# Kernel tuning notes

Measured on AMD Instinct MI355X. Metric: run time of the kernel, lower is better.

Reference implementation:

```python
import jax, jax.numpy as jnp
import numpy as np

NEG = -1000000.0  # same finite mask value as the Triton kernel


def setup_inputs() -> dict:
    key = jax.random.key(0)
    k1, k2, k3, k4 = jax.random.split(key, 4)
    B, H, KVH, S, D = 1, 32, 8, 2048, 128
    return {
        "q": jax.random.normal(k1, (B, H, S, D), dtype=jnp.float32),
        "k": jax.random.normal(k2, (B, KVH, S, D), dtype=jnp.float32),
        "v": jax.random.normal(k3, (B, KVH, S, D), dtype=jnp.float32),
        "sinks": jax.random.normal(k4, (H,), dtype=jnp.float32),
        "bandwidth": 1024,
    }


def reference(q, k, v, sinks, bandwidth):
    """Prefill flash attention with causal + sliding-window masking, GQA, and
    per-head attention sinks (extra logit in the softmax denominator)."""
    B, H, S, D = q.shape
    ratio = H // k.shape[1]  # KV_HEAD_RATIO
    kf = jnp.repeat(k, ratio, axis=1)  # [B,H,S,D]
    vf = jnp.repeat(v, ratio, axis=1)
    sm_scale = 1.0 / np.sqrt(D).astype(np.float32)

    logits = jnp.einsum("bhqd,bhkd->bhqk", q, kf) * sm_scale  # [B,H,S,S]
    q_pos = jnp.arange(S)[:, None]
    k_pos = jnp.arange(S)[None, :]
    mask = k_pos > q_pos  # causal
    if bandwidth > 0:
        mask = mask | (k_pos < q_pos - bandwidth + 1)  # sliding window
    logits = jnp.where(mask, NEG, logits)

    sink = sinks[None, :, None]  # [1,H,1] broadcast over batch, query
    m = jnp.maximum(jnp.max(logits, axis=-1), sink)  # [B,H,S]
    p = jnp.exp(logits - m[..., None])
    denom = p.sum(axis=-1) + jnp.exp(sink - m)  # sink contributes to denom only
    out = jnp.einsum("bhqk,bhkd->bhqd", p, vf) / denom[..., None]
    return out
```

## Files before the change

### kernel.cpp

```cpp
#include <hip/hip_runtime.h>
#include <hip/hip_bf16.h>

typedef __bf16 bf16x8 __attribute__((ext_vector_type(8)));
typedef unsigned short u16x8 __attribute__((ext_vector_type(8)));
typedef unsigned int u32x4 __attribute__((ext_vector_type(4)));
typedef float f32x4 __attribute__((ext_vector_type(4)));

#define SLEN 2048
#define DDIM 128
#define NH   32
#define NKVH 8
#define KVB  32
#define MINIT  -1e30f
#define MASKED -3e30f
#define LOG2E  1.4426950408889634f

static __device__ __forceinline__ unsigned short f2bfu(float f) {
  union { float f; unsigned u; } x; x.f = f;
  return (unsigned short)((x.u + 0x7fffu + ((x.u >> 16) & 1u)) >> 16);
}
static __device__ __forceinline__ float bfu2f(unsigned short u) {
  union { unsigned u; float f; } x; x.u = ((unsigned)u) << 16;
  return x.f;
}
static __device__ __forceinline__ unsigned cvt_pk_bf16(float lo, float hi) {
  unsigned r;
  asm("v_cvt_pk_bf16_f32 %0, %1, %2" : "=v"(r) : "v"(lo), "v"(hi));
  return r;
}
static __device__ __forceinline__ f32x4 mfma_bf16(u16x8 a, u16x8 b, f32x4 c) {
  return __builtin_amdgcn_mfma_f32_16x16x32_bf16(
      __builtin_bit_cast(bf16x8, a), __builtin_bit_cast(bf16x8, b), c, 0, 0, 0);
}
static __device__ __forceinline__ int vswz_k(int row) {
  return (row & 3) | (((row >> 3) & 1) << 2);
}

__global__ __launch_bounds__(256) void conv_kv(const float* __restrict__ k,
                                               const float* __restrict__ v,
                                               unsigned* __restrict__ kdst,
                                               unsigned short* __restrict__ vt) {
  __shared__ unsigned T32[32][17];
  const int bb = blockIdx.x;
  if (bb < 1024) {
    const int i = bb * 256 + threadIdx.x;
    const float4 f0 = ((const float4*)k)[2 * i];
    const float4 f1 = ((const float4*)k)[2 * i + 1];
    u32x4 o = { cvt_pk_bf16(f0.x, f0.y), cvt_pk_bf16(f0.z, f0.w),
                cvt_pk_bf16(f1.x, f1.y), cvt_pk_bf16(f1.z, f1.w) };
    ((u32x4*)kdst)[i] = o;
    return;
  }
  const int b   = bb - 1024;
  const int dt  = b & 3;
  const int st  = (b >> 2) & 63;
  const int kvh = b >> 8;
  const int r  = threadIdx.x >> 3;
  const int cg = threadIdx.x & 7;
  const float4 f = *(const float4*)(v + ((size_t)(kvh * SLEN + st * 32 + r) * DDIM) + dt * 32 + cg * 4);
  T32[r][cg * 2]     = cvt_pk_bf16(f.x, f.y);
  T32[r][cg * 2 + 1] = cvt_pk_bf16(f.z, f.w);
  __syncthreads();
  const int dr = threadIdx.x >> 3;
  const unsigned sel = (dr & 1) ? 0x07060302u : 0x05040100u;
  const unsigned a0 = T32[cg * 4 + 0][dr >> 1], a1 = T32[cg * 4 + 1][dr >> 1];
  const unsigned a2 = T32[cg * 4 + 2][dr >> 1], a3 = T32[cg * 4 + 3][dr >> 1];
  unsigned short* vp = vt + (size_t)kvh * DDIM * SLEN + (size_t)(dt * 32 + dr) * SLEN + st * 32 + cg * 4;
  const unsigned w0 = __builtin_amdgcn_perm(a1, a0, sel);
  const unsigned w1 = __builtin_amdgcn_perm(a3, a2, sel);
  vp[0] = (unsigned short)(w0 & 0xffff);
  vp[1] = (unsigned short)(w0 >> 16);
  vp[2] = (unsigned short)(w1 & 0xffff);
  vp[3] = (unsigned short)(w1 >> 16);
}

template <int NCH>
__global__ __launch_bounds__(256, 4) void attn_fwd(
    const float* __restrict__ q, const unsigned short* __restrict__ kbf,
    const unsigned short* __restrict__ vtg, const float* __restrict__ sinks,
    const int* __restrict__ bwp, float* __restrict__ out,
    unsigned short* __restrict__ pO, float* __restrict__ pm,
    float* __restrict__ pl) {
  constexpr int NQT = 32;
  __shared__ unsigned short Kl[KVB * DDIM];
  __shared__ unsigned short Vt[DDIM * KVB];
  __shared__ float SmS[4][16];

  const int tid  = threadIdx.x;
  const int wid  = tid >> 6;
  const int lane = tid & 63;
  const int ln   = lane & 15;
  const int hi   = lane >> 4;

  const int B   = blockIdx.x;
  const int x   = B & 7;
  const int j   = B >> 3;
  constexpr int per = 4 * NCH;
  const int qt  = NQT - 1 - (j / per);
  const int rem = j % per;
  const int hh  = rem / NCH;
  const int c   = rem % NCH;
  const int h   = x * 4 + hh;
  const int kvh = x;
  const int q0  = qt * 64;
  const int qrow0 = q0 + wid * 16;
  const int qpos  = qrow0 + ln;

  const int bwv    = bwp[0];
  const int lo_off = (bwv > 0) ? (bwv - 1) : SLEN;

  const int T0 = max(0, q0 - lo_off) >> 5;
  const int T1 = (q0 + 63) >> 5;
  const int N  = T1 - T0 + 1;
  const int ch = (N + NCH - 1) / NCH;
  const int Ts = T0 + c * ch;
  const int Te = min(T1, Ts + ch - 1);

  const float c2 = 0.08838834764831845f * LOG2E;

  u16x8 qf[4];
  {
    const float* qp = q + ((size_t)(h * SLEN + qpos) * DDIM) + hi * 8;
    #pragma unroll
    for (int dk = 0; dk < 4; ++dk) {
      float4 f0 = *(const float4*)(qp + dk * 32);
      float4 f1 = *(const float4*)(qp + dk * 32 + 4);
      u32x4 t = { cvt_pk_bf16(f0.x, f0.y), cvt_pk_bf16(f0.z, f0.w),
                  cvt_pk_bf16(f1.x, f1.y), cvt_pk_bf16(f1.z, f1.w) };
      qf[dk] = __builtin_bit_cast(u16x8, t);
    }
  }

  float m2 = MINIT;
  float l_ln = 0.0f;
  f32x4 oacc[8];
  #pragma unroll
  for (int nt = 0; nt < 8; ++nt) oacc[nt] = f32x4{0.f, 0.f, 0.f, 0.f};

  const unsigned short* Kg = kbf + (size_t)kvh * SLEN * DDIM;
  const unsigned short* Vg = vtg + (size_t)kvh * DDIM * SLEN;

  const int kr0 = tid >> 4, sk = tid & 15;
  const int kr1 = kr0 + 16;
  const int kw0 = kr0 * DDIM + (((sk & 8) | ((sk & 7) ^ vswz_k(kr0))) * 8);
  const int kw1 = kr1 * DDIM + (((sk & 8) | ((sk & 7) ^ vswz_k(kr1))) * 8);
  const int vr0 = tid >> 2, sv = tid & 3;
  const int vr1 = vr0 + 64;
  const int vw0 = vr0 * KVB + ((sv ^ ((vr0 >> 1) & 3)) * 8);
  const int vw1 = vr1 * KVB + ((sv ^ ((vr1 >> 1) & 3)) * 8);

  const int prow = ((ln >> 2) << 3) | (ln & 3);
  const int vk   = (ln & 3) | (((ln >> 2) & 1) << 2);
  int kfo[4];
  #pragma unroll
  for (int dk = 0; dk < 4; ++dk) {
    const int s = dk * 4 + hi;
    kfo[dk] = prow * DDIM + (((s & 8) | ((s & 7) ^ vk)) * 8);
  }
  const int vro = ln * KVB + ((hi ^ ((ln >> 1) & 3)) * 8);

  if (Ts <= Te) {
    const int kbS = Ts * 32, kbE = Te * 32;

    u16x8 pk0, pk1, pv0, pv1;
    {
      pk0 = *(const u16x8*)(Kg + (size_t)(kbS + kr0) * DDIM + sk * 8);
      pk1 = *(const u16x8*)(Kg + (size_t)(kbS + kr1) * DDIM + sk * 8);
      pv0 = *(const u16x8*)(Vg + (size_t)vr0 * SLEN + kbS + sv * 8);
      pv1 = *(const u16x8*)(Vg + (size_t)vr1 * SLEN + kbS + sv * 8);
    }

    for (int kb = kbS; kb <= kbE; kb += KVB) {
      __syncthreads();
      *(u16x8*)&Kl[kw0] = pk0;
      *(u16x8*)&Kl[kw1] = pk1;
      *(u16x8*)&Vt[vw0] = pv0;
      *(u16x8*)&Vt[vw1] = pv1;
      __syncthreads();

      {
        const int nb = min(kb + KVB, kbE);
        pk0 = *(const u16x8*)(Kg + (size_t)(nb + kr0) * DDIM + sk * 8);
        pk1 = *(const u16x8*)(Kg + (size_t)(nb + kr1) * DDIM + sk * 8);
        pv0 = *(const u16x8*)(Vg + (size_t)vr0 * SLEN + nb + sv * 8);
        pv1 = *(const u16x8*)(Vg + (size_t)vr1 * SLEN + nb + sv * 8);
      }

      if (kb > qrow0 + 15) continue;
      if (kb + KVB - 1 < qrow0 - lo_off) continue;

      f32x4 sacc0 = {0,0,0,0}, sacc1 = {0,0,0,0};
      __builtin_amdgcn_s_setprio(1);
      #pragma unroll
      for (int dk = 0; dk < 4; ++dk) {
        sacc0 = mfma_bf16(*(const u16x8*)&Kl[kfo[dk]], qf[dk], sacc0);
        sacc1 = mfma_bf16(*(const u16x8*)&Kl[kfo[dk] + 4 * DDIM], qf[dk], sacc1);
      }
      __builtin_amdgcn_s_setprio(0);

      float p[8];
      const bool interior = (kb + KVB - 1 <= qrow0) && (kb >= qrow0 + 15 - lo_off);
      if (interior) {
        #pragma unroll
        for (int r = 0; r < 4; ++r) {
          p[r]     = sacc0[r] * c2;
          p[4 + r] = sacc1[r] * c2;
        }
      } else {
        #pragma unroll
        for (int r = 0; r < 4; ++r) {
          const int kp0 = kb + hi * 8 + r;
          const int kp1 = kp0 + 4;
          p[r]     = ((kp0 <= qpos) && (kp0 >= qpos - lo_off)) ? sacc0[r] * c2 : MASKED;
          p[4 + r] = ((kp1 <= qpos) && (kp1 >= qpos - lo_off)) ? sacc1[r] * c2 : MASKED;
        }
      }

      float mx = fmaxf(fmaxf(fmaxf(p[0], p[1]), fmaxf(p[2], p[3])),
                       fmaxf(fmaxf(p[4], p[5]), fmaxf(p[6], p[7])));
      mx = fmaxf(mx, __shfl_xor(mx, 16));
      mx = fmaxf(mx, __shfl_xor(mx, 32));

      if (__any(mx > m2 + 11.5415605f)) {
        const float mn   = fmaxf(m2, mx);
        const float corr = exp2f(m2 - mn);
        l_ln *= corr;
        m2 = mn;
        if (hi == 0) SmS[wid][ln] = corr;
        float c4[4];
        #pragma unroll
        for (int r = 0; r < 4; ++r) c4[r] = SmS[wid][hi * 4 + r];
        #pragma unroll
        for (int nt = 0; nt < 8; ++nt)
          #pragma unroll
          for (int r = 0; r < 4; ++r) oacc[nt][r] *= c4[r];
      }

      float s = 0.0f;
      #pragma unroll
      for (int jj = 0; jj < 8; ++jj) { p[jj] = exp2f(p[jj] - m2); s += p[jj]; }
      l_ln += s;

      const u32x4 paw = { cvt_pk_bf16(p[0], p[1]), cvt_pk_bf16(p[2], p[3]),
                          cvt_pk_bf16(p[4], p[5]), cvt_pk_bf16(p[6], p[7]) };
      const u16x8 pa = __builtin_bit_cast(u16x8, paw);

      __builtin_amdgcn_s_setprio(1);
      #pragma unroll
      for (int nt = 0; nt < 8; ++nt) {
        const u16x8 vb = *(const u16x8*)&Vt[vro + nt * 16 * KVB];
        oacc[nt] = mfma_bf16(pa, vb, oacc[nt]);
      }
      __builtin_amdgcn_s_setprio(0);
    }
  }

  l_ln += __shfl_xor(l_ln, 16);
  l_ln += __shfl_xor(l_ln, 32);

  if (NCH == 1) {
    const float sk2 = sinks[h] * LOG2E;
    const float M  = fmaxf(m2, sk2);
    const float ed = exp2f(m2 - M);
    const float fac_ln = ed / (l_ln * ed + exp2f(sk2 - M));
    if (hi == 0) SmS[wid][ln] = fac_ln;
    float fac4[4];
    #pragma unroll
    for (int r = 0; r < 4; ++r) fac4[r] = SmS[wid][hi * 4 + r];
    #pragma unroll
    for (int r = 0; r < 4; ++r) {
      float* op = out + ((size_t)(h * SLEN + qrow0 + hi*4 + r) * DDIM) + ln;
      #pragma unroll
      for (int nt = 0; nt < 8; ++nt) op[nt * 16] = oacc[nt][r] * fac4[r];
    }
  } else {
    const size_t Lb = ((size_t)(h * NQT + qt)) * NCH + c;
    if (hi == 0) {
      pm[Lb * 64 + wid * 16 + ln] = m2;
      pl[Lb * 64 + wid * 16 + ln] = l_ln;
    }
    #pragma unroll
    for (int r = 0; r < 4; ++r) {
      unsigned short* po = pO + (Lb * 64 + wid * 16 + hi * 4 + r) * 128 + ln;
      #pragma unroll
      for (int nt = 0; nt < 8; ++nt) po[nt * 16] = f2bfu(oacc[nt][r]);
    }
  }
}

template <int NCH, int QBLK, int NQT>
__global__ __launch_bounds__(256) void mergeN(
    const unsigned short* __restrict__ pO, const float* __restrict__ pm,
    const float* __restrict__ pl, const float* __restrict__ sinks,
    float* __restrict__ out) {
  const int b   = blockIdx.x;
  const int x   = b & 7;
  const int jj2 = b >> 3;
  const int h   = x * 4 + (jj2 >> 5);
  const int sub = jj2 & 31;
  const int rloc = sub * 64 + (threadIdx.x >> 2);
  const int rid  = h * 2048 + rloc;
  const int d0   = (threadIdx.x & 3) * 32;
  const int qt   = rloc / QBLK;
  const int lr   = rloc % QBLK;
  const size_t base = ((size_t)(h * NQT + qt) * NCH) * QBLK + lr;
  const float sk2 = sinks[h] * LOG2E;
  float mc[NCH], lc[NCH];
  float M = sk2;
  #pragma unroll
  for (int c = 0; c < NCH; ++c) {
    mc[c] = pm[base + (size_t)c * QBLK];
    lc[c] = pl[base + (size_t)c * QBLK];
    M = fmaxf(M, mc[c]);
  }
  float denom = exp2f(sk2 - M);
  float sc[NCH];
  #pragma unroll
  for (int c = 0; c < NCH; ++c) { sc[c] = exp2f(mc[c] - M); denom += lc[c] * sc[c]; }
  const float inv = 1.0f / denom;
  float o[32];
  #pragma unroll
  for (int i = 0; i < 32; ++i) o[i] = 0.f;
  #pragma unroll
  for (int c = 0; c < NCH; ++c) {
    const unsigned short* pp = pO + (base + (size_t)c * QBLK) * 128 + d0;
    const float s = sc[c] * inv;
    #pragma unroll
    for (int i = 0; i < 4; ++i) {
      u16x8 a = *(const u16x8*)(pp + i * 8);
      #pragma unroll
      for (int jj = 0; jj < 8; ++jj) o[i*8+jj] += bfu2f(a[jj]) * s;
    }
  }
  float* op = out + (size_t)rid * 128 + d0;
  #pragma unroll
  for (int i = 0; i < 8; ++i)
    *(float4*)(op + i*4) = make_float4(o[i*4], o[i*4+1], o[i*4+2], o[i*4+3]);
}

extern "C" void kernel_launch(void* const* d_in, const int* in_sizes, int n_in,
                              void* d_out, int out_size, void* d_ws, size_t ws_size,
                              hipStream_t stream) {
  const float* q     = (const float*)d_in[0];
  const float* k     = (const float*)d_in[1];
  const float* v     = (const float*)d_in[2];
  const float* sinks = (const float*)d_in[3];
  const int*   bw    = (const int*)d_in[4];
  float* out = (float*)d_out;

  const size_t kvElems = (size_t)NKVH * SLEN * DDIM;
  unsigned short* kbf = (unsigned short*)d_ws;
  unsigned short* vtg = kbf + kvElems;
  unsigned short* pO  = vtg + kvElems;

  const size_t nPart2 = (size_t)NH * 32 * 2 * 64;
  const size_t need2  = 4 * kvElems + nPart2 * 128 * 2 + nPart2 * 8;

  conv_kv<<<dim3(1024 + NKVH * 64 * 4), 256, 0, stream>>>(k, v, (unsigned*)kbf, vtg);

  if (ws_size >= need2) {
    float* pm = (float*)(pO + nPart2 * 128);
    float* pl = pm + nPart2;
    attn_fwd<2><<<dim3(2048), 256, 0, stream>>>(q, kbf, vtg, sinks, bw, out, pO, pm, pl);
    mergeN<2, 64, 32><<<dim3(1024), 256, 0, stream>>>(pO, pm, pl, sinks, out);
  } else {
    attn_fwd<1><<<dim3(1024), 256, 0, stream>>>(q, kbf, vtg, sinks, bw, out, pO, nullptr, nullptr);
  }
}
```

Baseline: 75.37 us.

## Switch attention to 32x32x16 MFMA with 128-row query tiles

Replaces the 16x16x32 bf16 MFMA tiling with 32x32x16 MFMA. Each wave now owns 32 query rows, so the block covers a 128-row query tile and the grid is halved. The K and V LDS layouts change to match the new operand format, and v_permlane32_swap repacks the P fragments for the PV product. The aim is to reuse each K/V tile across more query rows and issue fewer, larger MFMAs, at the cost of more registers (occupancy hint lowered from 4 to 2), fewer blocks and coarser causal/window tiles that waste more masked work.

```diff
diff --git a/kernel.cpp b/kernel.cpp
--- a/kernel.cpp
+++ b/kernel.cpp
@@ -4,7 +4,7 @@
 typedef __bf16 bf16x8 __attribute__((ext_vector_type(8)));
 typedef unsigned short u16x8 __attribute__((ext_vector_type(8)));
 typedef unsigned int u32x4 __attribute__((ext_vector_type(4)));
-typedef float f32x4 __attribute__((ext_vector_type(4)));
+typedef float f32x16 __attribute__((ext_vector_type(16)));
 
 #define SLEN 2048
 #define DDIM 128
@@ -28,12 +28,12 @@
   asm("v_cvt_pk_bf16_f32 %0, %1, %2" : "=v"(r) : "v"(lo), "v"(hi));
   return r;
 }
-static __device__ __forceinline__ f32x4 mfma_bf16(u16x8 a, u16x8 b, f32x4 c) {
-  return __builtin_amdgcn_mfma_f32_16x16x32_bf16(
+static __device__ __forceinline__ f32x16 mfma32(u16x8 a, u16x8 b, f32x16 c) {
+  return __builtin_amdgcn_mfma_f32_32x32x16_bf16(
       __builtin_bit_cast(bf16x8, a), __builtin_bit_cast(bf16x8, b), c, 0, 0, 0);
 }
-static __device__ __forceinline__ int vswz_k(int row) {
-  return (row & 3) | (((row >> 3) & 1) << 2);
+static __device__ __forceinline__ void plswap(unsigned &a, unsigned &b) {
+  asm volatile("v_permlane32_swap_b32 %0, %1" : "+v"(a), "+v"(b));
 }
 
 __global__ __launch_bounds__(256) void conv_kv(const float* __restrict__ k,
@@ -75,22 +75,23 @@
 }
 
 template <int NCH>
-__global__ __launch_bounds__(256, 4) void attn_fwd(
+__global__ __launch_bounds__(256, 2) void attn_fwd(
     const float* __restrict__ q, const unsigned short* __restrict__ kbf,
     const unsigned short* __restrict__ vtg, const float* __restrict__ sinks,
     const int* __restrict__ bwp, float* __restrict__ out,
     unsigned short* __restrict__ pO, float* __restrict__ pm,
     float* __restrict__ pl) {
-  constexpr int NQT = 32;
-  __shared__ unsigned short Kl[KVB * DDIM];
-  __shared__ unsigned short Vt[DDIM * KVB];
-  __shared__ float SmS[4][16];
+  constexpr int QBLK = 128;
+  constexpr int NQT  = SLEN / QBLK;
+  __shared__ unsigned short Kt[16 * 32 * 8];
+  __shared__ unsigned short Vt2[4 * 128 * 8];
+  __shared__ float SmS[4][32];
 
   const int tid  = threadIdx.x;
   const int wid  = tid >> 6;
   const int lane = tid & 63;
-  const int ln   = lane & 15;
-  const int hi   = lane >> 4;
+  const int qc   = lane & 31;
+  const int hf   = lane >> 5;
 
   const int B   = blockIdx.x;
   const int x   = B & 7;
@@ -102,15 +103,15 @@
   const int c   = rem % NCH;
   const int h   = x * 4 + hh;
   const int kvh = x;
-  const int q0  = qt * 64;
-  const int qrow0 = q0 + wid * 16;
-  const int qpos  = qrow0 + ln;
+  const int q0  = qt * QBLK;
+  const int qrow0 = q0 + wid * 32;
+  const int qpos  = qrow0 + qc;
 
   const int bwv    = bwp[0];
   const int lo_off = (bwv > 0) ? (bwv - 1) : SLEN;
 
   const int T0 = max(0, q0 - lo_off) >> 5;
-  const int T1 = (q0 + 63) >> 5;
+  const int T1 = (q0 + QBLK - 1) >> 5;
   const int N  = T1 - T0 + 1;
   const int ch = (N + NCH - 1) / NCH;
   const int Ts = T0 + c * ch;
@@ -118,13 +119,13 @@
 
   const float c2 = 0.08838834764831845f * LOG2E;
 
-  u16x8 qf[4];
+  u16x8 qf[8];
   {
-    const float* qp = q + ((size_t)(h * SLEN + qpos) * DDIM) + hi * 8;
-    #pragma unroll
-    for (int dk = 0; dk < 4; ++dk) {
-      float4 f0 = *(const float4*)(qp + dk * 32);
-      float4 f1 = *(const float4*)(qp + dk * 32 + 4);
+    const float* qp = q + ((size_t)(h * SLEN + qpos) * DDIM) + hf * 8;
+    #pragma unroll
+    for (int dk = 0; dk < 8; ++dk) {
+      float4 f0 = *(const float4*)(qp + dk * 16);
+      float4 f1 = *(const float4*)(qp + dk * 16 + 4);
       u32x4 t = { cvt_pk_bf16(f0.x, f0.y), cvt_pk_bf16(f0.z, f0.w),
                   cvt_pk_bf16(f1.x, f1.y), cvt_pk_bf16(f1.z, f1.w) };
       qf[dk] = __builtin_bit_cast(u16x8, t);
@@ -133,92 +134,83 @@
 
   float m2 = MINIT;
   float l_ln = 0.0f;
-  f32x4 oacc[8];
-  #pragma unroll
-  for (int nt = 0; nt < 8; ++nt) oacc[nt] = f32x4{0.f, 0.f, 0.f, 0.f};
+  f32x16 oacc[4];
+  #pragma unroll
+  for (int t = 0; t < 4; ++t)
+    #pragma unroll
+    for (int r = 0; r < 16; ++r) oacc[t][r] = 0.0f;
 
   const unsigned short* Kg = kbf + (size_t)kvh * SLEN * DDIM;
   const unsigned short* Vg = vtg + (size_t)kvh * DDIM * SLEN;
 
-  const int kr0 = tid >> 4, sk = tid & 15;
-  const int kr1 = kr0 + 16;
-  const int kw0 = kr0 * DDIM + (((sk & 8) | ((sk & 7) ^ vswz_k(kr0))) * 8);
-  const int kw1 = kr1 * DDIM + (((sk & 8) | ((sk & 7) ^ vswz_k(kr1))) * 8);
-  const int vr0 = tid >> 2, sv = tid & 3;
-  const int vr1 = vr0 + 64;
-  const int vw0 = vr0 * KVB + ((sv ^ ((vr0 >> 1) & 3)) * 8);
-  const int vw1 = vr1 * KVB + ((sv ^ ((vr1 >> 1) & 3)) * 8);
-
-  const int prow = ((ln >> 2) << 3) | (ln & 3);
-  const int vk   = (ln & 3) | (((ln >> 2) & 1) << 2);
-  int kfo[4];
-  #pragma unroll
-  for (int dk = 0; dk < 4; ++dk) {
-    const int s = dk * 4 + hi;
-    kfo[dk] = prow * DDIM + (((s & 8) | ((s & 7) ^ vk)) * 8);
-  }
-  const int vro = ln * KVB + ((hi ^ ((ln >> 1) & 3)) * 8);
+  const int i0 = tid, i1 = 256 + tid;
+  const int ks0 = i0 >> 5, kr0 = i0 & 31;
+  const int ks1 = i1 >> 5, kr1 = i1 & 31;
+  const int vs0 = i0 >> 7, vd0 = i0 & 127;
+  const int vs1 = i1 >> 7, vd1 = i1 & 127;
+  const int klo0 = ks0 * 256 + kr0 * 8, klo1 = ks1 * 256 + kr1 * 8;
+  const int vlo0 = vs0 * 1024 + vd0 * 8, vlo1 = vs1 * 1024 + vd1 * 8;
+
+  int kro[8];
+  #pragma unroll
+  for (int dk = 0; dk < 8; ++dk) kro[dk] = (dk * 2 + hf) * 256 + qc * 8;
 
   if (Ts <= Te) {
     const int kbS = Ts * 32, kbE = Te * 32;
 
     u16x8 pk0, pk1, pv0, pv1;
-    {
-      pk0 = *(const u16x8*)(Kg + (size_t)(kbS + kr0) * DDIM + sk * 8);
-      pk1 = *(const u16x8*)(Kg + (size_t)(kbS + kr1) * DDIM + sk * 8);
-      pv0 = *(const u16x8*)(Vg + (size_t)vr0 * SLEN + kbS + sv * 8);
-      pv1 = *(const u16x8*)(Vg + (size_t)vr1 * SLEN + kbS + sv * 8);
-    }
+    pk0 = *(const u16x8*)(Kg + (size_t)(kbS + kr0) * DDIM + ks0 * 8);
+    pk1 = *(const u16x8*)(Kg + (size_t)(kbS + kr1) * DDIM + ks1 * 8);
+    pv0 = *(const u16x8*)(Vg + (size_t)vd0 * SLEN + kbS + vs0 * 8);
+    pv1 = *(const u16x8*)(Vg + (size_t)vd1 * SLEN + kbS + vs1 * 8);
 
     for (int kb = kbS; kb <= kbE; kb += KVB) {
       __syncthreads();
-      *(u16x8*)&Kl[kw0] = pk0;
-      *(u16x8*)&Kl[kw1] = pk1;
-      *(u16x8*)&Vt[vw0] = pv0;
-      *(u16x8*)&Vt[vw1] = pv1;
+      *(u16x8*)&Kt[klo0]  = pk0;
+      *(u16x8*)&Kt[klo1]  = pk1;
+      *(u16x8*)&Vt2[vlo0] = pv0;
+      *(u16x8*)&Vt2[vlo1] = pv1;
       __syncthreads();
 
       {
         const int nb = min(kb + KVB, kbE);
-        pk0 = *(const u16x8*)(Kg + (size_t)(nb + kr0) * DDIM + sk * 8);
-        pk1 = *(const u16x8*)(Kg + (size_t)(nb + kr1) * DDIM + sk * 8);
-        pv0 = *(const u16x8*)(Vg + (size_t)vr0 * SLEN + nb + sv * 8);
-        pv1 = *(const u16x8*)(Vg + (size_t)vr1 * SLEN + nb + sv * 8);
+        pk0 = *(const u16x8*)(Kg + (size_t)(nb + kr0) * DDIM + ks0 * 8);
+        pk1 = *(const u16x8*)(Kg + (size_t)(nb + kr1) * DDIM + ks1 * 8);
+        pv0 = *(const u16x8*)(Vg + (size_t)vd0 * SLEN + nb + vs0 * 8);
+        pv1 = *(const u16x8*)(Vg + (size_t)vd1 * SLEN + nb + vs1 * 8);
       }
 
-      if (kb > qrow0 + 15) continue;
+      if (kb > qrow0 + 31) continue;
       if (kb + KVB - 1 < qrow0 - lo_off) continue;
 
-      f32x4 sacc0 = {0,0,0,0}, sacc1 = {0,0,0,0};
+      f32x16 sacc;
+      #pragma unroll
+      for (int r = 0; r < 16; ++r) sacc[r] = 0.0f;
       __builtin_amdgcn_s_setprio(1);
       #pragma unroll
-      for (int dk = 0; dk < 4; ++dk) {
-        sacc0 = mfma_bf16(*(const u16x8*)&Kl[kfo[dk]], qf[dk], sacc0);
-        sacc1 = mfma_bf16(*(const u16x8*)&Kl[kfo[dk] + 4 * DDIM], qf[dk], sacc1);
-      }
+      for (int dk = 0; dk < 8; ++dk)
+        sacc = mfma32(*(const u16x8*)&Kt[kro[dk]], qf[dk], sacc);
       __builtin_amdgcn_s_setprio(0);
 
-      float p[8];
-      const bool interior = (kb + KVB - 1 <= qrow0) && (kb >= qrow0 + 15 - lo_off);
+      float p[16];
+      const bool interior = (kb + KVB - 1 <= qrow0) && (kb >= qrow0 + 31 - lo_off);
       if (interior) {
         #pragma unroll
-        for (int r = 0; r < 4; ++r) {
-          p[r]     = sacc0[r] * c2;
-          p[4 + r] = sacc1[r] * c2;
-        }
+        for (int r = 0; r < 16; ++r) p[r] = sacc[r] * c2;
       } else {
         #pragma unroll
-        for (int r = 0; r < 4; ++r) {
-          const int kp0 = kb + hi * 8 + r;
-          const int kp1 = kp0 + 4;
-          p[r]     = ((kp0 <= qpos) && (kp0 >= qpos - lo_off)) ? sacc0[r] * c2 : MASKED;
-          p[4 + r] = ((kp1 <= qpos) && (kp1 >= qpos - lo_off)) ? sacc1[r] * c2 : MASKED;
-        }
+        for (int rq = 0; rq < 4; ++rq)
+          #pragma unroll
+          for (int ri = 0; ri < 4; ++ri) {
+            const int r  = rq * 4 + ri;
+            const int kp = kb + ri + 8 * rq + 4 * hf;
+            p[r] = ((kp <= qpos) && (kp >= qpos - lo_off)) ? sacc[r] * c2 : MASKED;
+          }
       }
 
-      float mx = fmaxf(fmaxf(fmaxf(p[0], p[1]), fmaxf(p[2], p[3])),
-                       fmaxf(fmaxf(p[4], p[5]), fmaxf(p[6], p[7])));
-      mx = fmaxf(mx, __shfl_xor(mx, 16));
+      float mx = p[0];
+      #pragma unroll
+      for (int r = 1; r < 16; ++r) mx = fmaxf(mx, p[r]);
       mx = fmaxf(mx, __shfl_xor(mx, 32));
 
       if (__any(mx > m2 + 11.5415605f)) {
@@ -226,64 +218,70 @@
         const float corr = exp2f(m2 - mn);
         l_ln *= corr;
         m2 = mn;
-        if (hi == 0) SmS[wid][ln] = corr;
-        float c4[4];
+        if (hf == 0) SmS[wid][qc] = corr;
         #pragma unroll
-        for (int r = 0; r < 4; ++r) c4[r] = SmS[wid][hi * 4 + r];
-        #pragma unroll
-        for (int nt = 0; nt < 8; ++nt)
+        for (int r = 0; r < 16; ++r) {
+          const float cr = SmS[wid][(r & 3) + 8 * (r >> 2) + 4 * hf];
           #pragma unroll
-          for (int r = 0; r < 4; ++r) oacc[nt][r] *= c4[r];
+          for (int t = 0; t < 4; ++t) oacc[t][r] *= cr;
+        }
       }
 
       float s = 0.0f;
       #pragma unroll
-      for (int jj = 0; jj < 8; ++jj) { p[jj] = exp2f(p[jj] - m2); s += p[jj]; }
+      for (int r = 0; r < 16; ++r) { p[r] = exp2f(p[r] - m2); s += p[r]; }
       l_ln += s;
 
-      const u32x4 paw = { cvt_pk_bf16(p[0], p[1]), cvt_pk_bf16(p[2], p[3]),
-                          cvt_pk_bf16(p[4], p[5]), cvt_pk_bf16(p[6], p[7]) };
-      const u16x8 pa = __builtin_bit_cast(u16x8, paw);
+      unsigned A0 = cvt_pk_bf16(p[0],  p[1]),  A1 = cvt_pk_bf16(p[2],  p[3]);
+      unsigned B0 = cvt_pk_bf16(p[4],  p[5]),  B1 = cvt_pk_bf16(p[6],  p[7]);
+      unsigned C0 = cvt_pk_bf16(p[8],  p[9]),  C1 = cvt_pk_bf16(p[10], p[11]);
+      unsigned D0 = cvt_pk_bf16(p[12], p[13]), D1 = cvt_pk_bf16(p[14], p[15]);
+      plswap(A0, B0); plswap(A1, B1);
+      plswap(C0, D0); plswap(C1, D1);
+      const u16x8 a0 = __builtin_bit_cast(u16x8, u32x4{A0, A1, B0, B1});
+      const u16x8 a1 = __builtin_bit_cast(u16x8, u32x4{C0, C1, D0, D1});
 
       __builtin_amdgcn_s_setprio(1);
       #pragma unroll
-      for (int nt = 0; nt < 8; ++nt) {
-        const u16x8 vb = *(const u16x8*)&Vt[vro + nt * 16 * KVB];
-        oacc[nt] = mfma_bf16(pa, vb, oacc[nt]);
+      for (int t = 0; t < 4; ++t) {
+        const u16x8 vb0 = *(const u16x8*)&Vt2[(0 * 2 + hf) * 1024 + (t * 32 + qc) * 8];
+        oacc[t] = mfma32(a0, vb0, oacc[t]);
+        const u16x8 vb1 = *(const u16x8*)&Vt2[(1 * 2 + hf) * 1024 + (t * 32 + qc) * 8];
+        oacc[t] = mfma32(a1, vb1, oacc[t]);
       }
       __builtin_amdgcn_s_setprio(0);
     }
   }
 
-  l_ln += __shfl_xor(l_ln, 16);
   l_ln += __shfl_xor(l_ln, 32);
 
   if (NCH == 1) {
     const float sk2 = sinks[h] * LOG2E;
     const float M  = fmaxf(m2, sk2);
     const float ed = exp2f(m2 - M);
-    const float fac_ln = ed / (l_ln * ed + exp2f(sk2 - M));
-    if (hi == 0) SmS[wid][ln] = fac_ln;
-    float fac4[4];
-    #pragma unroll
-    for (int r = 0; r < 4; ++r) fac4[r] = SmS[wid][hi * 4 + r];
-    #pragma unroll
-    for (int r = 0; r < 4; ++r) {
-      float* op = out + ((size_t)(h * SLEN + qrow0 + hi*4 + r) * DDIM) + ln;
-      #pragma unroll
-      for (int nt = 0; nt < 8; ++nt) op[nt * 16] = oacc[nt][r] * fac4[r];
+    const float fac = ed / (l_ln * ed + exp2f(sk2 - M));
+    if (hf == 0) SmS[wid][qc] = fac;
+    __builtin_amdgcn_s_barrier();
+    #pragma unroll
+    for (int r = 0; r < 16; ++r) {
+      const int qr = (r & 3) + 8 * (r >> 2) + 4 * hf;
+      const float fr = SmS[wid][qr];
+      float* op = out + ((size_t)(h * SLEN + qrow0 + qr) * DDIM) + qc;
+      #pragma unroll
+      for (int t = 0; t < 4; ++t) op[t * 32] = oacc[t][r] * fr;
     }
   } else {
     const size_t Lb = ((size_t)(h * NQT + qt)) * NCH + c;
-    if (hi == 0) {
-      pm[Lb * 64 + wid * 16 + ln] = m2;
-      pl[Lb * 64 + wid * 16 + ln] = l_ln;
-    }
-    #pragma unroll
-    for (int r = 0; r < 4; ++r) {
-      unsigned short* po = pO + (Lb * 64 + wid * 16 + hi * 4 + r) * 128 + ln;
-      #pragma unroll
-      for (int nt = 0; nt < 8; ++nt) po[nt * 16] = f2bfu(oacc[nt][r]);
+    if (hf == 0) {
+      pm[Lb * QBLK + wid * 32 + qc] = m2;
+      pl[Lb * QBLK + wid * 32 + qc] = l_ln;
+    }
+    #pragma unroll
+    for (int r = 0; r < 16; ++r) {
+      const int qr = (r & 3) + 8 * (r >> 2) + 4 * hf;
+      unsigned short* po = pO + (Lb * QBLK + wid * 32 + qr) * 128 + qc;
+      #pragma unroll
+      for (int t = 0; t < 4; ++t) po[t * 32] = f2bfu(oacc[t][r]);
     }
   }
 }
@@ -293,6 +291,7 @@
     const unsigned short* __restrict__ pO, const float* __restrict__ pm,
     const float* __restrict__ pl, const float* __restrict__ sinks,
     float* __restrict__ out) {
+  typedef unsigned short u16x8 __attribute__((ext_vector_type(8)));
   const int b   = blockIdx.x;
   const int x   = b & 7;
   const int jj2 = b >> 3;
@@ -353,7 +352,7 @@
   unsigned short* vtg = kbf + kvElems;
   unsigned short* pO  = vtg + kvElems;
 
-  const size_t nPart2 = (size_t)NH * 32 * 2 * 64;
+  const size_t nPart2 = (size_t)NH * 16 * 2 * 128;
   const size_t need2  = 4 * kvElems + nPart2 * 128 * 2 + nPart2 * 8;
 
   conv_kv<<<dim3(1024 + NKVH * 64 * 4), 256, 0, stream>>>(k, v, (unsigned*)kbf, vtg);
@@ -361,9 +360,9 @@
   if (ws_size >= need2) {
     float* pm = (float*)(pO + nPart2 * 128);
     float* pl = pm + nPart2;
-    attn_fwd<2><<<dim3(2048), 256, 0, stream>>>(q, kbf, vtg, sinks, bw, out, pO, pm, pl);
-    mergeN<2, 64, 32><<<dim3(1024), 256, 0, stream>>>(pO, pm, pl, sinks, out);
+    attn_fwd<2><<<dim3(1024), 256, 0, stream>>>(q, kbf, vtg, sinks, bw, out, pO, pm, pl);
+    mergeN<2, 128, 16><<<dim3(1024), 256, 0, stream>>>(pO, pm, pl, sinks, out);
   } else {
-    attn_fwd<1><<<dim3(1024), 256, 0, stream>>>(q, kbf, vtg, sinks, bw, out, pO, nullptr, nullptr);
-  }
-}
+    attn_fwd<1><<<dim3(512), 256, 0, stream>>>(q, kbf, vtg, sinks, bw, out, pO, nullptr, nullptr);
+  }
+}
```

Measured after the change: 77.64 us. +3.0%, slower.
